# Performance work log

Measured on AMD Instinct MI355X. Metric: run time of the kernel, lower is better.

## Reference

```python
import jax, jax.numpy as jnp
import numpy as np

B, C, H, W = 4, 96, 64, 64
N_STATE, DT_RANK, K = 16, 6, 3


def _layernorm(x, g, b, eps=1e-5):
    m = jnp.mean(x, axis=-1, keepdims=True)
    v = jnp.mean((x - m) ** 2, axis=-1, keepdims=True)
    return (x - m) / jnp.sqrt(v + eps) * g + b


def _grid_sample(img, gx, gy):
    # F.grid_sample: bilinear, align_corners=True, zeros padding; gx,gy in [-1,1], [B,Ho,Wo]
    Bc, Cc, Hi, Wi = img.shape
    fx = (gx + 1.0) * 0.5 * (Wi - 1)
    fy = (gy + 1.0) * 0.5 * (Hi - 1)
    x0 = jnp.floor(fx)
    y0 = jnp.floor(fy)
    wx1 = fx - x0
    wy1 = fy - y0

    def tap(ix, iy, w):
        valid = ((ix >= 0) & (ix < Wi) & (iy >= 0) & (iy < Hi)).astype(img.dtype)
        ic = jnp.clip(ix, 0, Wi - 1).astype(jnp.int32)
        jc = jnp.clip(iy, 0, Hi - 1).astype(jnp.int32)
        v = jax.vmap(lambda im, yy, xx: im[:, yy, xx])(img, jc, ic)  # [B,C,Ho,Wo]
        return v * (w * valid)[:, None, :, :]

    return (tap(x0, y0, (1 - wx1) * (1 - wy1)) + tap(x0 + 1, y0, wx1 * (1 - wy1))
            + tap(x0, y0 + 1, (1 - wx1) * wy1) + tap(x0 + 1, y0 + 1, wx1 * wy1))


def _resize_bilinear(img, Ho, Wo):
    # torch F.interpolate(mode='bilinear', align_corners=False)
    Bc, Cc, Hi, Wi = img.shape

    def src(n_out, n_in):
        s = jnp.maximum((jnp.arange(n_out, dtype=img.dtype) + 0.5) * (n_in / n_out) - 0.5, 0.0)
        i0 = jnp.floor(s).astype(jnp.int32)
        i1 = jnp.minimum(i0 + 1, n_in - 1)
        return i0, i1, s - i0

    y0, y1, wy = src(Ho, Hi)
    x0, x1, wx = src(Wo, Wi)
    row = img[:, :, y0, :] * (1 - wy)[None, None, :, None] + img[:, :, y1, :] * wy[None, None, :, None]
    return row[:, :, :, x0] * (1 - wx) + row[:, :, :, x1] * wx


def _conv_offset(x, conv1_w, conv1_b, ca1_w, ca1_b, ca2_w, ca2_b, ln_g, ln_b, conv2_w):
    Bc, Cc = x.shape[:2]
    p = conv1_w.shape[-1] // 2
    x1 = jax.lax.conv_general_dilated(
        x, conv1_w, (1, 1), [(p, p), (p, p)],
        dimension_numbers=("NCHW", "OIHW", "NCHW"), feature_group_count=Cc
    ) + conv1_b[None, :, None, None]
    xc = jnp.mean(x, axis=(2, 3))  # adaptive_avg_pool2d -> (1,1)
    hid = jax.nn.gelu(xc @ ca1_w.T + ca1_b, approximate=False)
    ca = jax.nn.sigmoid(hid @ ca2_w.T + ca2_b)
    x1 = x1 * ca[:, :, None, None]
    xn = _layernorm(jnp.transpose(x1, (0, 2, 3, 1)), ln_g, ln_b)
    xg = jax.nn.gelu(jnp.transpose(xn, (0, 3, 1, 2)), approximate=False)
    return jnp.einsum("bchw,oc->bohw", xg, conv2_w[:, :, 0, 0])


def _deformable(x, rpe_table, conv1_w, conv1_b, ca1_w, ca1_b, ca2_w, ca2_b, ln_g, ln_b, conv2_w):
    Bc, Cc, Hc, Wc = x.shape
    L = Hc * Wc
    off = _conv_offset(x, conv1_w, conv1_b, ca1_w, ca1_b, ca2_w, ca2_b, ln_g, ln_b, conv2_w)
    offset = off[:, :2]
    de = off[:, 2]
    rng = jnp.array([1.0 / (Hc - 1.0), 1.0 / (Wc - 1.0)], off.dtype).reshape(1, 2, 1, 1)
    offset = jnp.transpose(jnp.tanh(offset) * rng, (0, 2, 3, 1))  # [B,H,W,2] (dy,dx)
    ry = (jnp.linspace(0.5, Hc - 0.5, Hc) / (Hc - 1.0)) * 2.0 - 1.0
    rx = (jnp.linspace(0.5, Wc - 0.5, Wc) / (Wc - 1.0)) * 2.0 - 1.0
    ref = jnp.stack(jnp.meshgrid(ry, rx, indexing="ij"), -1)  # [H,W,2] (y,x)
    pos = offset + ref[None]
    de_index = jnp.tanh(de).reshape(Bc, L)
    path_ref = (jnp.linspace(0.5, L - 0.5, L) / (L - 1.0)) * 2.0 - 1.0
    path_pos = de_index + path_ref[None]
    x_sampled = _grid_sample(x, pos[..., 1], pos[..., 0])
    rpe = jnp.broadcast_to(rpe_table[None], (Bc,) + rpe_table.shape)
    rpe_bias = _resize_bilinear(rpe, Hc, Wc)
    ky = (jnp.linspace(0.0, float(Hc), Hc) / (Hc - 1.0)) * 2.0 - 1.0
    kx = (jnp.linspace(0.0, float(Wc), Wc) / (Wc - 1.0)) * 2.0 - 1.0
    key_grid = jnp.stack(jnp.meshgrid(ky, kx, indexing="ij"), -1)
    disp = (key_grid[None] - pos) * 0.5
    pos_bias = _grid_sample(rpe_bias, disp[..., 1], disp[..., 0])
    xd = (x_sampled + pos_bias).reshape(Bc, Cc, L)
    indices = jnp.argsort(path_pos, axis=-1)  # topk(k=N, largest=False) == ascending argsort
    xs2 = jnp.take_along_axis(xd, indices[:, None, :], axis=2)
    return xs2, indices


def _selective_scan(u, delta, A, Bs, Cs, Dv, delta_bias):
    Bc, KD, L = u.shape
    Kk = Bs.shape[1]
    Dd = KD // Kk
    Ns = A.shape[1]
    delta = jax.nn.softplus(delta + delta_bias[None, :, None])
    dt4 = jnp.moveaxis(delta.reshape(Bc, Kk, Dd, L), 3, 0)
    u4 = jnp.moveaxis(u.reshape(Bc, Kk, Dd, L), 3, 0)
    Bt = jnp.moveaxis(Bs, 3, 0)
    Ct = jnp.moveaxis(Cs, 3, 0)
    A3 = A.reshape(Kk, Dd, Ns)

    @jax.checkpoint
    def step(h, inp):
        dt, ut, bt, ct = inp  # [B,K,D],[B,K,D],[B,K,N],[B,K,N]
        h = jnp.exp(dt[..., None] * A3) * h + (dt * ut)[..., None] * bt[:, :, None, :]
        return h, jnp.einsum("bkdn,bkn->bkd", h, ct)

    h0 = jnp.zeros((Bc, Kk, Dd, Ns), u.dtype)
    _, ys = jax.lax.scan(step, h0, (dt4, u4, Bt, Ct))
    ys = jnp.moveaxis(ys, 0, 3).reshape(Bc, KD, L)
    return ys + u * Dv[None, :, None]


def _forward(x, x_proj_weight, dt_projs_weight, dt_projs_bias, A_logs, Ds_param,
             conv1_w, conv1_b, ca1_w, ca1_b, ca2_w, ca2_b, ln_g, ln_b, conv2_w, rpe_table):
    Bc, Dd, Hc, Wc = x.shape
    L = Hc * Wc
    Kk, _, R = dt_projs_weight.shape
    Ns = A_logs.shape[1]
    xs0 = x.reshape(Bc, Dd, L)
    xs2, indices = _deformable(x, rpe_table, conv1_w, conv1_b, ca1_w, ca1_b, ca2_w, ca2_b, ln_g, ln_b, conv2_w)
    xs = jnp.stack([xs0, xs0[..., ::-1], xs2], axis=1)  # [B,3,D,L]
    x_dbl = jnp.einsum("bkdl,kcd->bkcl", xs, x_proj_weight)
    dts, Bs, Cs = jnp.split(x_dbl, [R, R + Ns], axis=2)
    dts = jnp.einsum("bkrl,kdr->bkdl", dts, dt_projs_weight)
    A = -jnp.exp(A_logs)
    ys = _selective_scan(xs.reshape(Bc, Kk * Dd, L), dts.reshape(Bc, Kk * Dd, L),
                         A, Bs, Cs, Ds_param, dt_projs_bias.reshape(-1))
    ys = ys.reshape(Bc, Kk, Dd, L)
    inv = jnp.argsort(indices, axis=-1)  # inverse permutation (DeformableLayerReverse)
    y2 = jnp.take_along_axis(ys[:, 2], inv[:, None, :], axis=2)
    y = (ys[:, 0] + ys[:, 1][..., ::-1] + y2) / 3.0
    return jnp.transpose(y, (0, 2, 1)).reshape(Bc, Hc, Wc, Dd)


def setup_inputs():
    key = jax.random.key(0)
    ks = jax.random.split(key, 12)
    f = jnp.float32
    return {
        "x": jax.random.normal(ks[0], (B, C, H, W), f),
        "x_proj_weight": jax.random.normal(ks[1], (K, DT_RANK + 2 * N_STATE, C), f) * 0.05,
        "dt_projs_weight": jax.random.normal(ks[2], (K, C, DT_RANK), f) * 0.05,
        "dt_projs_bias": jax.random.normal(ks[3], (K, C), f) * 0.1,
        "A_logs": jnp.tile(jnp.log(jnp.arange(1, N_STATE + 1, dtype=f))[None, :], (K * C, 1)),
        "Ds_param": jnp.ones((K * C,), f),
        "conv1_w": jax.random.normal(ks[4], (C, 1, 9, 9), f) * 0.05,
        "conv1_b": jnp.zeros((C,), f),
        "ca1_w": jax.random.normal(ks[5], (C // 16, C), f) * 0.1,
        "ca1_b": jnp.zeros((C // 16,), f),
        "ca2_w": jax.random.normal(ks[6], (C, C // 16), f) * 0.1,
        "ca2_b": jnp.zeros((C,), f),
        "ln_g": jnp.ones((C,), f),
        "ln_b": jnp.zeros((C,), f),
        "conv2_w": jax.random.normal(ks[7], (3, C, 1, 1), f) * 0.05,
        "rpe_table": jax.random.normal(ks[8], (C, 7, 7), f) * 0.01,
    }


def reference(x, x_proj_weight, dt_projs_weight, dt_projs_bias, A_logs, Ds_param,
              conv1_w, conv1_b, ca1_w, ca1_b, ca2_w, ca2_b, ln_g, ln_b, conv2_w, rpe_table):
    return _forward(x, x_proj_weight, dt_projs_weight, dt_projs_bias, A_logs, Ds_param,
                    conv1_w, conv1_b, ca1_w, ca1_b, ca2_w, ca2_b, ln_g, ln_b, conv2_w, rpe_table)
```

## Files before the change

kernel.cpp:

```cpp
#include <hip/hip_runtime.h>

#define BB 4
#define CC 96
#define HH 64
#define WW 64
#define LL 4096
#define KK 3
#define RR 6
#define NN 16

__device__ __forceinline__ float geluf(float x){
    return 0.5f * x * (1.0f + erff(x * 0.70710678118654752f));
}
__device__ __forceinline__ float softplusf(float x){
    return fmaxf(x, 0.0f) + log1pf(expf(-fabsf(x)));
}
__device__ __forceinline__ float sigmoidf(float x){
    return 1.0f / (1.0f + expf(-x));
}

__global__ __launch_bounds__(256) void k_mean(const float* __restrict__ x, float* __restrict__ xc){
    int bc = blockIdx.x;
    const float* p = x + (size_t)bc * LL;
    float s = 0.f;
    for (int i = threadIdx.x; i < LL; i += 256) s += p[i];
    __shared__ float red[256];
    red[threadIdx.x] = s; __syncthreads();
    for (int st = 128; st > 0; st >>= 1){
        if (threadIdx.x < st) red[threadIdx.x] += red[threadIdx.x + st];
        __syncthreads();
    }
    if (threadIdx.x == 0) xc[bc] = red[0] * (1.0f / LL);
}

__global__ __launch_bounds__(128) void k_ca(const float* __restrict__ xc,
                     const float* __restrict__ w1, const float* __restrict__ b1,
                     const float* __restrict__ w2, const float* __restrict__ b2,
                     float* __restrict__ ca){
    int b = blockIdx.x;
    int t = threadIdx.x;
    __shared__ float hid[CC/16];
    if (t < CC/16){
        float a = b1[t];
        for (int d = 0; d < CC; d++) a += w1[t*CC + d] * xc[b*CC + d];
        hid[t] = geluf(a);
    }
    __syncthreads();
    if (t < CC){
        float a = b2[t];
        #pragma unroll
        for (int i = 0; i < CC/16; i++) a += w2[t*(CC/16) + i] * hid[i];
        ca[b*CC + t] = sigmoidf(a);
    }
}

__global__ __launch_bounds__(256) void k_conv(const float* __restrict__ x, const float* __restrict__ w,
                       const float* __restrict__ bias, const float* __restrict__ ca,
                       float* __restrict__ x1){
    int gid = blockIdx.x * 256 + threadIdx.x;
    int l = gid & (LL-1); int bc = gid >> 12;
    int c = bc % CC; int b = bc / CC;
    int h = l >> 6, wq = l & 63;
    const float* xp = x + (size_t)bc * LL;
    const float* wp = w + c * 81;
    float acc = 0.f;
    #pragma unroll
    for (int ky = 0; ky < 9; ky++){
        int yy = h + ky - 4;
        if (yy < 0 || yy >= HH) continue;
        #pragma unroll
        for (int kx = 0; kx < 9; kx++){
            int xx = wq + kx - 4;
            if (xx < 0 || xx >= WW) continue;
            acc += xp[yy*WW + xx] * wp[ky*9 + kx];
        }
    }
    x1[gid] = (acc + bias[c]) * ca[b*CC + c];
}

__global__ __launch_bounds__(256) void k_rpe(const float* __restrict__ t, float* __restrict__ out){
    int gid = blockIdx.x * 256 + threadIdx.x;
    int l = gid & (LL-1); int c = gid >> 12;
    int h = l >> 6, w = l & 63;
    float sy = fmaxf((h + 0.5f) * (7.0f/64.0f) - 0.5f, 0.f);
    float sx = fmaxf((w + 0.5f) * (7.0f/64.0f) - 0.5f, 0.f);
    int y0 = (int)floorf(sy); int x0 = (int)floorf(sx);
    float wy = sy - (float)y0, wx = sx - (float)x0;
    int y1 = min(y0 + 1, 6), x1i = min(x0 + 1, 6);
    const float* tp = t + c * 49;
    float r0 = tp[y0*7 + x0] * (1.f - wy) + tp[y1*7 + x0] * wy;
    float r1 = tp[y0*7 + x1i] * (1.f - wy) + tp[y1*7 + x1i] * wy;
    out[gid] = r0 * (1.f - wx) + r1 * wx;
}

__global__ __launch_bounds__(256) void k_off(const float* __restrict__ x1,
                      const float* __restrict__ g, const float* __restrict__ bta,
                      const float* __restrict__ w2,
                      float* __restrict__ posy, float* __restrict__ posx, float* __restrict__ path){
    int blk = blockIdx.x;
    int ltile = blk & 63; int b = blk >> 6;
    int lane = threadIdx.x & 63;
    int wg = threadIdx.x >> 6;
    int l = ltile * 64 + lane;
    const float* p = x1 + (size_t)b * CC * LL + l;
    float v[24];
    float s = 0.f, ss = 0.f;
    #pragma unroll
    for (int j = 0; j < 24; j++){
        float t = p[(size_t)(wg*24 + j) * LL];
        v[j] = t; s += t; ss += t*t;
    }
    __shared__ float ls[4][64], lss[4][64];
    ls[wg][lane] = s; lss[wg][lane] = ss;
    __syncthreads();
    s  = ls[0][lane]  + ls[1][lane]  + ls[2][lane]  + ls[3][lane];
    ss = lss[0][lane] + lss[1][lane] + lss[2][lane] + lss[3][lane];
    float m = s * (1.0f/CC);
    float rstd = rsqrtf(ss*(1.0f/CC) - m*m + 1e-5f);
    float a0 = 0.f, a1 = 0.f, a2 = 0.f;
    #pragma unroll
    for (int j = 0; j < 24; j++){
        int c = wg*24 + j;
        float xn = (v[j]-m)*rstd*g[c] + bta[c];
        float xg = geluf(xn);
        a0 = fmaf(w2[c],      xg, a0);
        a1 = fmaf(w2[CC+c],   xg, a1);
        a2 = fmaf(w2[2*CC+c], xg, a2);
    }
    __shared__ float la[3][4][64];
    la[0][wg][lane] = a0; la[1][wg][lane] = a1; la[2][wg][lane] = a2;
    __syncthreads();
    if (wg < 3){
        float a = la[wg][0][lane] + la[wg][1][lane] + la[wg][2][lane] + la[wg][3][lane];
        int h = l >> 6, w = l & 63;
        if (wg == 0)      posy[b*LL + l] = tanhf(a)*(1.0f/63.0f) + ((2*h+1)*(1.0f/63.0f) - 1.0f);
        else if (wg == 1) posx[b*LL + l] = tanhf(a)*(1.0f/63.0f) + ((2*w+1)*(1.0f/63.0f) - 1.0f);
        else              path[b*LL + l] = tanhf(a) + ((l + 0.5f)*(2.0f/4095.0f) - 1.0f);
    }
}

typedef unsigned long long u64s;
__device__ __forceinline__ u64s shflx64(u64s x, int m){
    int lo = __shfl_xor((int)(unsigned)x, m);
    int hi = __shfl_xor((int)(unsigned)(x >> 32), m);
    return ((u64s)(unsigned)hi << 32) | (unsigned)lo;
}
__device__ __forceinline__ void cex(u64s& a, u64s& b, bool up){
    u64s mn = a < b ? a : b;
    u64s mx = a < b ? b : a;
    a = up ? mn : mx;
    b = up ? mx : mn;
}
__global__ __launch_bounds__(1024) void k_sort(const float* __restrict__ path,
                                               int* __restrict__ idx, int* __restrict__ inv){
    int b = blockIdx.x;
    int t = threadIdx.x;
    __shared__ u64s lds[LL];
    u64s v[4];
    #pragma unroll
    for (int r = 0; r < 4; r++){
        int e = t*4 + r;
        unsigned u = __float_as_uint(path[b*LL + e]);
        u ^= (u >> 31) ? 0xFFFFFFFFu : 0x80000000u;
        v[r] = ((u64s)u << 32) | (unsigned)e;
    }
    for (int kk = 2; kk <= LL; kk <<= 1){
        for (int j = kk >> 1; j > 0; j >>= 1){
            if (j >= 256){
                __syncthreads();
                #pragma unroll
                for (int r = 0; r < 4; r++) lds[t*4 + r] = v[r];
                __syncthreads();
                #pragma unroll
                for (int r = 0; r < 4; r++){
                    int e = t*4 + r;
                    u64s pv = lds[e ^ j];
                    bool up    = ((e & kk) == 0);
                    bool lower = ((e & j) == 0);
                    u64s mn = v[r] < pv ? v[r] : pv;
                    u64s mx = v[r] < pv ? pv : v[r];
                    v[r] = (up == lower) ? mn : mx;
                }
            } else if (j >= 4){
                int m = j >> 2;
                #pragma unroll
                for (int r = 0; r < 4; r++){
                    u64s pv = shflx64(v[r], m);
                    bool up    = (((t*4 + r) & kk) == 0);
                    bool lower = ((t & m) == 0);
                    u64s mn = v[r] < pv ? v[r] : pv;
                    u64s mx = v[r] < pv ? pv : v[r];
                    v[r] = (up == lower) ? mn : mx;
                }
            } else if (j == 2){
                bool up = (((t*4) & kk) == 0);
                cex(v[0], v[2], up);
                cex(v[1], v[3], up);
            } else {
                if (kk == 2){
                    cex(v[0], v[1], true);
                    cex(v[2], v[3], false);
                } else {
                    bool up = (((t*4) & kk) == 0);
                    cex(v[0], v[1], up);
                    cex(v[2], v[3], up);
                }
            }
        }
    }
    #pragma unroll
    for (int r = 0; r < 4; r++){
        int e = t*4 + r;
        int id = (int)(unsigned)(v[r] & 0xFFFFFFFFu);
        idx[b*LL + e] = id;
        inv[b*LL + id] = e;
    }
}

__device__ __forceinline__ float bilin0(const float* __restrict__ img, float gx, float gy){
    float fx = (gx + 1.f) * 31.5f;
    float fy = (gy + 1.f) * 31.5f;
    float x0f = floorf(fx), y0f = floorf(fy);
    float wx = fx - x0f, wy = fy - y0f;
    int x0 = (int)x0f, y0 = (int)y0f;
    float acc = 0.f;
    bool vx0 = (x0 >= 0) & (x0 < WW), vx1 = (x0+1 >= 0) & (x0+1 < WW);
    bool vy0 = (y0 >= 0) & (y0 < HH), vy1 = (y0+1 >= 0) & (y0+1 < HH);
    if (vy0 & vx0) acc += img[y0*WW + x0]       * (1.f-wx) * (1.f-wy);
    if (vy0 & vx1) acc += img[y0*WW + x0+1]     * wx       * (1.f-wy);
    if (vy1 & vx0) acc += img[(y0+1)*WW + x0]   * (1.f-wx) * wy;
    if (vy1 & vx1) acc += img[(y0+1)*WW + x0+1] * wx       * wy;
    return acc;
}

__global__ __launch_bounds__(256) void k_sample(const float* __restrict__ x, const float* __restrict__ rpe,
                         const float* __restrict__ posy, const float* __restrict__ posx,
                         float* __restrict__ xd){
    int gid = blockIdx.x * 256 + threadIdx.x;
    int l = gid & (LL-1); int bc = gid >> 12;
    int b = bc / CC; int c = bc % CC;
    float gy = posy[b*LL + l], gx = posx[b*LL + l];
    float v = bilin0(x + (size_t)bc * LL, gx, gy);
    int h = l >> 6, w = l & 63;
    float ky = h * (128.0f/3969.0f) - 1.0f;
    float kx = w * (128.0f/3969.0f) - 1.0f;
    float v2 = bilin0(rpe + (size_t)c * LL, (kx - gx) * 0.5f, (ky - gy) * 0.5f);
    xd[gid] = v + v2;
}

__global__ __launch_bounds__(192, 1) void k_proj(const float* __restrict__ x, const float* __restrict__ xd,
    const int* __restrict__ indices, const float* __restrict__ xpw, const float* __restrict__ dtw,
    const float* __restrict__ dtb, float* __restrict__ u2, float* __restrict__ dt,
    float* __restrict__ Bst, float* __restrict__ Cst){
    int blk = blockIdx.x;
    int ltile = blk & 63; int bk = blk >> 6;
    int k = bk % KK; int b = bk / KK;
    int lane = threadIdx.x & 63;
    int w = threadIdx.x >> 6;
    const float* __restrict__ Wk = xpw + k*38*CC;
    int l = ltile * 64 + lane;
    int srcl = (k == 0) ? l : (k == 1 ? (LL-1-l) : indices[b*LL + l]);
    const float* xp = (k == 2 ? xd : x) + (size_t)b * CC * LL + srcl;

    __shared__ float vsh[CC*64];
    #pragma unroll
    for (int j = 0; j < 32; j++){
        int d = w*32 + j;
        vsh[d*64 + lane] = xp[(size_t)d * LL];
    }
    __syncthreads();

    if (w == 0){
        float acc[RR];
        #pragma unroll
        for (int i = 0; i < RR; i++) acc[i] = 0.f;
        for (int d = 0; d < CC; d++){
            float vv = vsh[d*64 + lane];
            #pragma unroll
            for (int i = 0; i < RR; i++) acc[i] = fmaf(Wk[i*CC + d], vv, acc[i]);
        }
        const float* __restrict__ Dw = dtw + k*CC*RR;
        const float* __restrict__ Db = dtb + k*CC;
        float* dtp = dt + (size_t)bk * CC * LL + l;
        #pragma unroll 8
        for (int d = 0; d < CC; d++){
            float sdt = Db[d];
            #pragma unroll
            for (int r = 0; r < RR; r++) sdt = fmaf(acc[r], Dw[d*RR + r], sdt);
            dtp[(size_t)d * LL] = softplusf(sdt);
        }
    } else if (w == 1){
        float acc[NN];
        #pragma unroll
        for (int i = 0; i < NN; i++) acc[i] = 0.f;
        for (int d = 0; d < CC; d++){
            float vv = vsh[d*64 + lane];
            #pragma unroll
            for (int i = 0; i < NN; i++) acc[i] = fmaf(Wk[(RR + i)*CC + d], vv, acc[i]);
        }
        size_t base = ((size_t)bk * LL + l) * NN;
        #pragma unroll
        for (int q = 0; q < 4; q++){
            float4 o; o.x = acc[q*4]; o.y = acc[q*4+1]; o.z = acc[q*4+2]; o.w = acc[q*4+3];
            *(float4*)(Bst + base + q*4) = o;
        }
    } else {
        float acc[NN];
        #pragma unroll
        for (int i = 0; i < NN; i++) acc[i] = 0.f;
        for (int d = 0; d < CC; d++){
            float vv = vsh[d*64 + lane];
            #pragma unroll
            for (int i = 0; i < NN; i++) acc[i] = fmaf(Wk[(RR + NN + i)*CC + d], vv, acc[i]);
        }
        size_t base = ((size_t)bk * LL + l) * NN;
        #pragma unroll
        for (int q = 0; q < 4; q++){
            float4 o; o.x = acc[q*4]; o.y = acc[q*4+1]; o.z = acc[q*4+2]; o.w = acc[q*4+3];
            *(float4*)(Cst + base + q*4) = o;
        }
        if (k == 2){
            float* up = u2 + (size_t)b * CC * LL + l;
            #pragma unroll 8
            for (int d = 0; d < CC; d++) up[(size_t)d * LL] = vsh[d*64 + lane];
        }
    }
}

#define SEG 128
#define TL 32
#define SROW 17
#define DROW 36
template<int KIND>
__device__ __forceinline__ void scan_body(int b, int d, const float* __restrict__ usrc,
    const float* __restrict__ dt, const float* __restrict__ Bst, const float* __restrict__ Cst,
    const float* __restrict__ Alog, const float* __restrict__ Ds, float* __restrict__ ys,
    float* sA, float* sB, float* sdt){
    int bk = b * KK + KIND;
    int tid = threadIdx.x;
    int ng = tid & 3;
    int seg = tid >> 2;
    int t0 = seg * TL;

    const float4 A4 = *(const float4*)(Alog + (KIND*CC + d)*NN + 4*ng);
    float A[4] = { -__expf(A4.x), -__expf(A4.y), -__expf(A4.z), -__expf(A4.w) };
    float Dv = Ds[KIND*CC + d];

    const float* dtp = dt + ((size_t)bk * CC + d) * LL + t0;
    const float* ub = (KIND == 1)
        ? usrc + ((size_t)b*CC + d) * LL + (LL-4-t0)
        : usrc + ((size_t)b*CC + d) * LL + t0;
    const float* Bp = Bst + ((size_t)bk * LL + t0) * NN + 4*ng;
    const float* Cp = Cst + ((size_t)bk * LL + t0) * NN + 4*ng;
    float* yp = ys + ((size_t)bk * CC + d) * LL + t0;

    float Ap[4] = {1.f,1.f,1.f,1.f}, h[4] = {0.f,0.f,0.f,0.f};
    for (int t = 0; t < TL; t += 4){
        float4 dq = *(const float4*)(dtp + t);
        float4 uq = (KIND == 1) ? *(const float4*)(ub - t) : *(const float4*)(ub + t);
        float dd[4] = {dq.x, dq.y, dq.z, dq.w};
        float uu[4];
        if (KIND == 1){ uu[0]=uq.w; uu[1]=uq.z; uu[2]=uq.y; uu[3]=uq.x; }
        else          { uu[0]=uq.x; uu[1]=uq.y; uu[2]=uq.z; uu[3]=uq.w; }
        if (ng == 0) *(float4*)(sdt + seg*DROW + t) = dq;
        #pragma unroll
        for (int i = 0; i < 4; i++){
            float4 Bq = *(const float4*)(Bp + (t+i)*NN);
            float du = dd[i] * uu[i];
            float bb[4] = {Bq.x, Bq.y, Bq.z, Bq.w};
            #pragma unroll
            for (int j = 0; j < 4; j++){
                float a = __expf(dd[i] * A[j]);
                Ap[j] *= a;
                h[j] = fmaf(a, h[j], du * bb[j]);
            }
        }
    }

    #pragma unroll
    for (int j = 0; j < 4; j++){
        sA[seg*SROW + 4*ng + j] = Ap[j];
        sB[seg*SROW + 4*ng + j] = h[j];
    }
    __syncthreads();
    {
        int wv = tid >> 6;
        int lane = tid & 63;
        #pragma unroll
        for (int nn = 0; nn < 2; nn++){
            int n = 2*wv + nn;
            float a1 = sA[(2*lane)*SROW + n],   b1 = sB[(2*lane)*SROW + n];
            float a2 = sA[(2*lane+1)*SROW + n], b2 = sB[(2*lane+1)*SROW + n];
            float ca = a1 * a2;
            float cb = fmaf(a2, b1, b2);
            #pragma unroll
            for (int off = 1; off < 64; off <<= 1){
                float ta = __shfl_up(ca, off);
                float tb = __shfl_up(cb, off);
                if (lane >= off){
                    cb = fmaf(ca, tb, cb);
                    ca *= ta;
                }
            }
            float cb_prev = __shfl_up(cb, 1);
            if (lane == 0) cb_prev = 0.f;
            sA[(2*lane)*SROW + n]   = cb_prev;
            sA[(2*lane+1)*SROW + n] = fmaf(a1, cb_prev, b1);
        }
    }
    __syncthreads();
    float hc[4];
    #pragma unroll
    for (int j = 0; j < 4; j++) hc[j] = sA[seg*SROW + 4*ng + j];

    for (int t = 0; t < TL; t += 4){
        float4 dq = *(const float4*)(sdt + seg*DROW + t);
        float4 uq = (KIND == 1) ? *(const float4*)(ub - t) : *(const float4*)(ub + t);
        float dd[4] = {dq.x, dq.y, dq.z, dq.w};
        float uu[4];
        if (KIND == 1){ uu[0]=uq.w; uu[1]=uq.z; uu[2]=uq.y; uu[3]=uq.x; }
        else          { uu[0]=uq.x; uu[1]=uq.y; uu[2]=uq.z; uu[3]=uq.w; }
        float yo[4];
        #pragma unroll
        for (int i = 0; i < 4; i++){
            float4 Bq = *(const float4*)(Bp + (t+i)*NN);
            float4 Cq = *(const float4*)(Cp + (t+i)*NN);
            float du = dd[i] * uu[i];
            float bb[4] = {Bq.x, Bq.y, Bq.z, Bq.w};
            float cc[4] = {Cq.x, Cq.y, Cq.z, Cq.w};
            float p = 0.f;
            #pragma unroll
            for (int j = 0; j < 4; j++){
                float a = __expf(dd[i] * A[j]);
                hc[j] = fmaf(a, hc[j], du * bb[j]);
                p = fmaf(hc[j], cc[j], p);
            }
            p += __shfl_xor(p, 1);
            p += __shfl_xor(p, 2);
            yo[i] = fmaf(uu[i], Dv, p);
        }
        if (ng == 0){
            float4 o; o.x = yo[0]; o.y = yo[1]; o.z = yo[2]; o.w = yo[3];
            *(float4*)(yp + t) = o;
        }
    }
}

__global__ __launch_bounds__(512) void k_scan_all(const float* __restrict__ x, const float* __restrict__ u2,
    const float* __restrict__ dt, const float* __restrict__ Bst, const float* __restrict__ Cst,
    const float* __restrict__ Alog, const float* __restrict__ Ds, float* __restrict__ ys){
    __shared__ float sA[SEG*SROW];
    __shared__ float sB[SEG*SROW];
    __shared__ float sdt[SEG*DROW];
    int blk = blockIdx.x;
    int k = blk / (BB*CC);
    int r = blk % (BB*CC);
    int d = r % CC; int b = r / CC;
    if (k == 0)      scan_body<0>(b, d, x,  dt, Bst, Cst, Alog, Ds, ys, sA, sB, sdt);
    else if (k == 1) scan_body<1>(b, d, x,  dt, Bst, Cst, Alog, Ds, ys, sA, sB, sdt);
    else             scan_body<2>(b, d, u2, dt, Bst, Cst, Alog, Ds, ys, sA, sB, sdt);
}

__global__ __launch_bounds__(256) void k_comb(const float* __restrict__ ys, const int* __restrict__ inv,
                                              float* __restrict__ out){
    int tile = blockIdx.x & 63; int b = blockIdx.x >> 6;
    int l0 = tile * 64;
    __shared__ float t0[CC * 65];
    __shared__ int invs[64];
    if (threadIdx.x < 64) invs[threadIdx.x] = inv[b*LL + l0 + threadIdx.x];
    __syncthreads();
    const float* y0p = ys + (size_t)(b*KK + 0) * CC * LL;
    const float* y1p = ys + (size_t)(b*KK + 1) * CC * LL;
    const float* y2p = ys + (size_t)(b*KK + 2) * CC * LL;
    for (int it = 0; it < 24; it++){
        int e = it * 256 + threadIdx.x;
        int li = e & 63; int c = e >> 6;
        int l = l0 + li;
        float v = y0p[(size_t)c*LL + l] + y1p[(size_t)c*LL + (LL-1-l)] + y2p[(size_t)c*LL + invs[li]];
        t0[c*65 + li] = v * (1.0f/3.0f);
    }
    __syncthreads();
    for (int it = 0; it < 24; it++){
        int e = it * 256 + threadIdx.x;
        int c = e % CC; int li = e / CC;
        out[((size_t)b*LL + l0 + li) * CC + c] = t0[c*65 + li];
    }
}

extern "C" void kernel_launch(void* const* d_in, const int* in_sizes, int n_in,
                              void* d_out, int out_size, void* d_ws, size_t ws_size,
                              hipStream_t stream){
    const float* x    = (const float*)d_in[0];
    const float* xpw  = (const float*)d_in[1];
    const float* dtw  = (const float*)d_in[2];
    const float* dtb  = (const float*)d_in[3];
    const float* Alog = (const float*)d_in[4];
    const float* Ds   = (const float*)d_in[5];
    const float* c1w  = (const float*)d_in[6];
    const float* c1b  = (const float*)d_in[7];
    const float* ca1w = (const float*)d_in[8];
    const float* ca1b = (const float*)d_in[9];
    const float* ca2w = (const float*)d_in[10];
    const float* ca2b = (const float*)d_in[11];
    const float* lng  = (const float*)d_in[12];
    const float* lnb  = (const float*)d_in[13];
    const float* c2w  = (const float*)d_in[14];
    const float* rpet = (const float*)d_in[15];
    float* out = (float*)d_out;

    float* ws   = (float*)d_ws;
    float* xc   = ws;
    float* ca   = xc + 384;
    float* x1   = ca + 384;
    float* rpe  = x1 + (size_t)BB*CC*LL;
    float* posy = rpe + (size_t)CC*LL;
    float* posx = posy + (size_t)BB*LL;
    float* path = posx + (size_t)BB*LL;
    float* xd   = path + (size_t)BB*LL;
    int*   idx  = (int*)(xd + (size_t)BB*CC*LL);
    int*   inv  = idx + (size_t)BB*LL;
    float* u2   = (float*)(inv + (size_t)BB*LL);
    float* dtA  = u2 + (size_t)BB*CC*LL;
    float* Bst  = dtA + (size_t)BB*KK*CC*LL;
    float* Cst  = Bst + (size_t)BB*KK*LL*NN;
    float* ysA  = Cst + (size_t)BB*KK*LL*NN;

    k_mean  <<<BB*CC, 256, 0, stream>>>(x, xc);
    k_ca    <<<BB, 128, 0, stream>>>(xc, ca1w, ca1b, ca2w, ca2b, ca);
    k_conv  <<<(BB*CC*LL)/256, 256, 0, stream>>>(x, c1w, c1b, ca, x1);
    k_rpe   <<<(CC*LL)/256, 256, 0, stream>>>(rpet, rpe);
    k_off   <<<BB*64, 256, 0, stream>>>(x1, lng, lnb, c2w, posy, posx, path);
    k_sort  <<<BB, 1024, 0, stream>>>(path, idx, inv);
    k_sample<<<(BB*CC*LL)/256, 256, 0, stream>>>(x, rpe, posy, posx, xd);
    k_proj  <<<BB*KK*64, 192, 0, stream>>>(x, xd, idx, xpw, dtw, dtb, u2, dtA, Bst, Cst);
    k_scan_all<<<KK*BB*CC, 512, 0, stream>>>(x, u2, dtA, Bst, Cst, Alog, Ds, ysA);
    k_comb  <<<BB*64, 256, 0, stream>>>(ysA, inv, out);
}
```

Baseline: 349.4 us.

## Split k_proj channel reduction across four lanes with shuffle reduction

```diff
diff --git a/kernel.cpp b/kernel.cpp
--- a/kernel.cpp
+++ b/kernel.cpp
@@ -248,82 +248,66 @@
     xd[gid] = v + v2;
 }
 
-__global__ __launch_bounds__(192, 1) void k_proj(const float* __restrict__ x, const float* __restrict__ xd,
+__global__ __launch_bounds__(64) void k_proj(const float* __restrict__ x, const float* __restrict__ xd,
     const int* __restrict__ indices, const float* __restrict__ xpw, const float* __restrict__ dtw,
     const float* __restrict__ dtb, float* __restrict__ u2, float* __restrict__ dt,
     float* __restrict__ Bst, float* __restrict__ Cst){
     int blk = blockIdx.x;
-    int ltile = blk & 63; int bk = blk >> 6;
+    int ltile = blk & 255; int bk = blk >> 8;
     int k = bk % KK; int b = bk / KK;
-    int lane = threadIdx.x & 63;
-    int w = threadIdx.x >> 6;
-    const float* __restrict__ Wk = xpw + k*38*CC;
-    int l = ltile * 64 + lane;
+    int lane = threadIdx.x;
+    int ll = lane >> 2;
+    int part = lane & 3;
+    int l = ltile * 16 + ll;
     int srcl = (k == 0) ? l : (k == 1 ? (LL-1-l) : indices[b*LL + l]);
     const float* xp = (k == 2 ? xd : x) + (size_t)b * CC * LL + srcl;
-
-    __shared__ float vsh[CC*64];
-    #pragma unroll
-    for (int j = 0; j < 32; j++){
-        int d = w*32 + j;
-        vsh[d*64 + lane] = xp[(size_t)d * LL];
-    }
-    __syncthreads();
-
-    if (w == 0){
-        float acc[RR];
-        #pragma unroll
-        for (int i = 0; i < RR; i++) acc[i] = 0.f;
-        for (int d = 0; d < CC; d++){
-            float vv = vsh[d*64 + lane];
-            #pragma unroll
-            for (int i = 0; i < RR; i++) acc[i] = fmaf(Wk[i*CC + d], vv, acc[i]);
-        }
-        const float* __restrict__ Dw = dtw + k*CC*RR;
-        const float* __restrict__ Db = dtb + k*CC;
-        float* dtp = dt + (size_t)bk * CC * LL + l;
-        #pragma unroll 8
-        for (int d = 0; d < CC; d++){
-            float sdt = Db[d];
-            #pragma unroll
-            for (int r = 0; r < RR; r++) sdt = fmaf(acc[r], Dw[d*RR + r], sdt);
-            dtp[(size_t)d * LL] = softplusf(sdt);
-        }
-    } else if (w == 1){
-        float acc[NN];
-        #pragma unroll
-        for (int i = 0; i < NN; i++) acc[i] = 0.f;
-        for (int d = 0; d < CC; d++){
-            float vv = vsh[d*64 + lane];
-            #pragma unroll
-            for (int i = 0; i < NN; i++) acc[i] = fmaf(Wk[(RR + i)*CC + d], vv, acc[i]);
-        }
-        size_t base = ((size_t)bk * LL + l) * NN;
-        #pragma unroll
-        for (int q = 0; q < 4; q++){
-            float4 o; o.x = acc[q*4]; o.y = acc[q*4+1]; o.z = acc[q*4+2]; o.w = acc[q*4+3];
-            *(float4*)(Bst + base + q*4) = o;
-        }
-    } else {
-        float acc[NN];
-        #pragma unroll
-        for (int i = 0; i < NN; i++) acc[i] = 0.f;
-        for (int d = 0; d < CC; d++){
-            float vv = vsh[d*64 + lane];
-            #pragma unroll
-            for (int i = 0; i < NN; i++) acc[i] = fmaf(Wk[(RR + NN + i)*CC + d], vv, acc[i]);
-        }
-        size_t base = ((size_t)bk * LL + l) * NN;
-        #pragma unroll
-        for (int q = 0; q < 4; q++){
-            float4 o; o.x = acc[q*4]; o.y = acc[q*4+1]; o.z = acc[q*4+2]; o.w = acc[q*4+3];
-            *(float4*)(Cst + base + q*4) = o;
-        }
-        if (k == 2){
-            float* up = u2 + (size_t)b * CC * LL + l;
-            #pragma unroll 8
-            for (int d = 0; d < CC; d++) up[(size_t)d * LL] = vsh[d*64 + lane];
-        }
+    const float* __restrict__ Wk = xpw + k*38*CC;
+
+    float v[24];
+    #pragma unroll
+    for (int j = 0; j < 24; j++) v[j] = xp[(size_t)(part*24 + j) * LL];
+
+    float acc[38];
+    #pragma unroll
+    for (int i = 0; i < 38; i++) acc[i] = 0.f;
+    #pragma unroll
+    for (int j = 0; j < 24; j++){
+        int d = part*24 + j;
+        #pragma unroll
+        for (int i = 0; i < 38; i++) acc[i] = fmaf(Wk[i*CC + d], v[j], acc[i]);
+    }
+    #pragma unroll
+    for (int i = 0; i < 38; i++){
+        acc[i] += __shfl_xor(acc[i], 1);
+        acc[i] += __shfl_xor(acc[i], 2);
+    }
+
+    size_t base = ((size_t)bk * LL + l) * NN;
+    {
+        float4 o;
+        o.x = acc[RR + 4*part + 0]; o.y = acc[RR + 4*part + 1];
+        o.z = acc[RR + 4*part + 2]; o.w = acc[RR + 4*part + 3];
+        *(float4*)(Bst + base + 4*part) = o;
+        float4 p2;
+        p2.x = acc[RR+NN + 4*part + 0]; p2.y = acc[RR+NN + 4*part + 1];
+        p2.z = acc[RR+NN + 4*part + 2]; p2.w = acc[RR+NN + 4*part + 3];
+        *(float4*)(Cst + base + 4*part) = p2;
+    }
+    if (k == 2){
+        float* up = u2 + (size_t)b * CC * LL + l;
+        #pragma unroll
+        for (int j = 0; j < 24; j++) up[(size_t)(part*24 + j) * LL] = v[j];
+    }
+    const float* __restrict__ Dw = dtw + k*CC*RR;
+    const float* __restrict__ Db = dtb + k*CC;
+    float* dtp = dt + (size_t)bk * CC * LL + l;
+    #pragma unroll 4
+    for (int j = 0; j < 24; j++){
+        int d = part*24 + j;
+        float sdt = Db[d];
+        #pragma unroll
+        for (int r = 0; r < RR; r++) sdt = fmaf(acc[r], Dw[d*RR + r], sdt);
+        dtp[(size_t)d * LL] = softplusf(sdt);
     }
 }
 
@@ -532,7 +516,7 @@
     k_off   <<<BB*64, 256, 0, stream>>>(x1, lng, lnb, c2w, posy, posx, path);
     k_sort  <<<BB, 1024, 0, stream>>>(path, idx, inv);
     k_sample<<<(BB*CC*LL)/256, 256, 0, stream>>>(x, rpe, posy, posx, xd);
-    k_proj  <<<BB*KK*64, 192, 0, stream>>>(x, xd, idx, xpw, dtw, dtb, u2, dtA, Bst, Cst);
+    k_proj  <<<BB*KK*256, 64, 0, stream>>>(x, xd, idx, xpw, dtw, dtb, u2, dtA, Bst, Cst);
     k_scan_all<<<KK*BB*CC, 512, 0, stream>>>(x, u2, dtA, Bst, Cst, Alog, Ds, ysA);
     k_comb  <<<BB*64, 256, 0, stream>>>(ysA, inv, out);
 }
```

After: 373.5 us. 1.07x slower.

## Repartition scan threads to 8 per segment with 2 states each, drop dt LDS cache

Applied to the files above, without the earlier changes.

```diff
diff --git a/kernel.cpp b/kernel.cpp
--- a/kernel.cpp
+++ b/kernel.cpp
@@ -327,34 +327,33 @@
     }
 }
 
-#define SEG 128
-#define TL 32
+#define SEG 64
+#define TL 64
 #define SROW 17
-#define DROW 36
 template<int KIND>
 __device__ __forceinline__ void scan_body(int b, int d, const float* __restrict__ usrc,
     const float* __restrict__ dt, const float* __restrict__ Bst, const float* __restrict__ Cst,
     const float* __restrict__ Alog, const float* __restrict__ Ds, float* __restrict__ ys,
-    float* sA, float* sB, float* sdt){
+    float* sA, float* sB){
     int bk = b * KK + KIND;
     int tid = threadIdx.x;
-    int ng = tid & 3;
-    int seg = tid >> 2;
+    int ng = tid & 7;
+    int seg = tid >> 3;
     int t0 = seg * TL;
 
-    const float4 A4 = *(const float4*)(Alog + (KIND*CC + d)*NN + 4*ng);
-    float A[4] = { -__expf(A4.x), -__expf(A4.y), -__expf(A4.z), -__expf(A4.w) };
+    const float2 A2 = *(const float2*)(Alog + (KIND*CC + d)*NN + 2*ng);
+    float A[2] = { -__expf(A2.x), -__expf(A2.y) };
     float Dv = Ds[KIND*CC + d];
 
     const float* dtp = dt + ((size_t)bk * CC + d) * LL + t0;
     const float* ub = (KIND == 1)
         ? usrc + ((size_t)b*CC + d) * LL + (LL-4-t0)
         : usrc + ((size_t)b*CC + d) * LL + t0;
-    const float* Bp = Bst + ((size_t)bk * LL + t0) * NN + 4*ng;
-    const float* Cp = Cst + ((size_t)bk * LL + t0) * NN + 4*ng;
+    const float* Bp = Bst + ((size_t)bk * LL + t0) * NN + 2*ng;
+    const float* Cp = Cst + ((size_t)bk * LL + t0) * NN + 2*ng;
     float* yp = ys + ((size_t)bk * CC + d) * LL + t0;
 
-    float Ap[4] = {1.f,1.f,1.f,1.f}, h[4] = {0.f,0.f,0.f,0.f};
+    float Ap[2] = {1.f,1.f}, h[2] = {0.f,0.f};
     for (int t = 0; t < TL; t += 4){
         float4 dq = *(const float4*)(dtp + t);
         float4 uq = (KIND == 1) ? *(const float4*)(ub - t) : *(const float4*)(ub + t);
@@ -362,25 +361,22 @@
         float uu[4];
         if (KIND == 1){ uu[0]=uq.w; uu[1]=uq.z; uu[2]=uq.y; uu[3]=uq.x; }
         else          { uu[0]=uq.x; uu[1]=uq.y; uu[2]=uq.z; uu[3]=uq.w; }
-        if (ng == 0) *(float4*)(sdt + seg*DROW + t) = dq;
         #pragma unroll
         for (int i = 0; i < 4; i++){
-            float4 Bq = *(const float4*)(Bp + (t+i)*NN);
+            float2 Bq = *(const float2*)(Bp + (t+i)*NN);
             float du = dd[i] * uu[i];
-            float bb[4] = {Bq.x, Bq.y, Bq.z, Bq.w};
-            #pragma unroll
-            for (int j = 0; j < 4; j++){
-                float a = __expf(dd[i] * A[j]);
-                Ap[j] *= a;
-                h[j] = fmaf(a, h[j], du * bb[j]);
-            }
-        }
-    }
-
-    #pragma unroll
-    for (int j = 0; j < 4; j++){
-        sA[seg*SROW + 4*ng + j] = Ap[j];
-        sB[seg*SROW + 4*ng + j] = h[j];
+            float a0 = __expf(dd[i] * A[0]);
+            float a1 = __expf(dd[i] * A[1]);
+            Ap[0] *= a0; Ap[1] *= a1;
+            h[0] = fmaf(a0, h[0], du * Bq.x);
+            h[1] = fmaf(a1, h[1], du * Bq.y);
+        }
+    }
+
+    #pragma unroll
+    for (int j = 0; j < 2; j++){
+        sA[seg*SROW + 2*ng + j] = Ap[j];
+        sB[seg*SROW + 2*ng + j] = h[j];
     }
     __syncthreads();
     {
@@ -389,10 +385,8 @@
         #pragma unroll
         for (int nn = 0; nn < 2; nn++){
             int n = 2*wv + nn;
-            float a1 = sA[(2*lane)*SROW + n],   b1 = sB[(2*lane)*SROW + n];
-            float a2 = sA[(2*lane+1)*SROW + n], b2 = sB[(2*lane+1)*SROW + n];
-            float ca = a1 * a2;
-            float cb = fmaf(a2, b1, b2);
+            float ca = sA[lane*SROW + n];
+            float cb = sB[lane*SROW + n];
             #pragma unroll
             for (int off = 1; off < 64; off <<= 1){
                 float ta = __shfl_up(ca, off);
@@ -404,17 +398,16 @@
             }
             float cb_prev = __shfl_up(cb, 1);
             if (lane == 0) cb_prev = 0.f;
-            sA[(2*lane)*SROW + n]   = cb_prev;
-            sA[(2*lane+1)*SROW + n] = fmaf(a1, cb_prev, b1);
-        }
-    }
-    __syncthreads();
-    float hc[4];
-    #pragma unroll
-    for (int j = 0; j < 4; j++) hc[j] = sA[seg*SROW + 4*ng + j];
+            sA[lane*SROW + n] = cb_prev;
+        }
+    }
+    __syncthreads();
+    float hc[2];
+    #pragma unroll
+    for (int j = 0; j < 2; j++) hc[j] = sA[seg*SROW + 2*ng + j];
 
     for (int t = 0; t < TL; t += 4){
-        float4 dq = *(const float4*)(sdt + seg*DROW + t);
+        float4 dq = *(const float4*)(dtp + t);
         float4 uq = (KIND == 1) ? *(const float4*)(ub - t) : *(const float4*)(ub + t);
         float dd[4] = {dq.x, dq.y, dq.z, dq.w};
         float uu[4];
@@ -423,20 +416,17 @@
         float yo[4];
         #pragma unroll
         for (int i = 0; i < 4; i++){
-            float4 Bq = *(const float4*)(Bp + (t+i)*NN);
-            float4 Cq = *(const float4*)(Cp + (t+i)*NN);
+            float2 Bq = *(const float2*)(Bp + (t+i)*NN);
+            float2 Cq = *(const float2*)(Cp + (t+i)*NN);
             float du = dd[i] * uu[i];
-            float bb[4] = {Bq.x, Bq.y, Bq.z, Bq.w};
-            float cc[4] = {Cq.x, Cq.y, Cq.z, Cq.w};
-            float p = 0.f;
-            #pragma unroll
-            for (int j = 0; j < 4; j++){
-                float a = __expf(dd[i] * A[j]);
-                hc[j] = fmaf(a, hc[j], du * bb[j]);
-                p = fmaf(hc[j], cc[j], p);
-            }
+            float a0 = __expf(dd[i] * A[0]);
+            float a1 = __expf(dd[i] * A[1]);
+            hc[0] = fmaf(a0, hc[0], du * Bq.x);
+            hc[1] = fmaf(a1, hc[1], du * Bq.y);
+            float p = fmaf(hc[1], Cq.y, hc[0] * Cq.x);
             p += __shfl_xor(p, 1);
             p += __shfl_xor(p, 2);
+            p += __shfl_xor(p, 4);
             yo[i] = fmaf(uu[i], Dv, p);
         }
         if (ng == 0){
@@ -451,14 +441,13 @@
     const float* __restrict__ Alog, const float* __restrict__ Ds, float* __restrict__ ys){
     __shared__ float sA[SEG*SROW];
     __shared__ float sB[SEG*SROW];
-    __shared__ float sdt[SEG*DROW];
     int blk = blockIdx.x;
     int k = blk / (BB*CC);
     int r = blk % (BB*CC);
     int d = r % CC; int b = r / CC;
-    if (k == 0)      scan_body<0>(b, d, x,  dt, Bst, Cst, Alog, Ds, ys, sA, sB, sdt);
-    else if (k == 1) scan_body<1>(b, d, x,  dt, Bst, Cst, Alog, Ds, ys, sA, sB, sdt);
-    else             scan_body<2>(b, d, u2, dt, Bst, Cst, Alog, Ds, ys, sA, sB, sdt);
+    if (k == 0)      scan_body<0>(b, d, x,  dt, Bst, Cst, Alog, Ds, ys, sA, sB);
+    else if (k == 1) scan_body<1>(b, d, x,  dt, Bst, Cst, Alog, Ds, ys, sA, sB);
+    else             scan_body<2>(b, d, u2, dt, Bst, Cst, Alog, Ds, ys, sA, sB);
 }
 
 __global__ __launch_bounds__(256) void k_comb(const float* __restrict__ ys, const int* __restrict__ inv,
```

Result: no change. 354.1 us (+1.4%).
